# Kernel optimization log

Hardware: AMD Instinct MI355X
Metric: run time of the kernel (lower is better)

## Reference

```python
import jax, jax.numpy as jnp
import numpy as np

H, BOTTLENECK, TOPK = 2048, 64, 128
TAU, EPS = 1.0, 1e-20

def setup_inputs() -> dict:
    key = jax.random.key(0)
    ks = jax.random.split(key, 7)
    B, T = 4, 4096
    x = jax.random.normal(ks[0], (B, T, H), dtype=jnp.float32)
    Wd = jax.random.normal(ks[1], (H, BOTTLENECK), dtype=jnp.float32) / np.sqrt(H)
    bd = jax.random.normal(ks[2], (BOTTLENECK,), dtype=jnp.float32) * 0.01
    Wu = jax.random.normal(ks[3], (BOTTLENECK, H), dtype=jnp.float32) / np.sqrt(BOTTLENECK)
    bu = jax.random.normal(ks[4], (H,), dtype=jnp.float32) * 0.01
    Wg = jax.random.normal(ks[5], (H,), dtype=jnp.float32) / np.sqrt(H)
    bg = jax.random.normal(ks[6], (), dtype=jnp.float32) * 0.01
    return {"x": x, "Wd": Wd, "bd": bd, "Wu": Wu, "bu": bu, "Wg": Wg, "bg": bg}

def reference(x, Wd, bd, Wu, bu, Wg, bg):
    B, T, _ = x.shape
    k = max(1, min(T, TOPK))
    # gate logits: Linear(H,1).squeeze(-1) -> [B, T]
    logits = jnp.einsum('bth,h->bt', x, Wg) + bg
    # gumbel noise (fixed key for determinism; non-differentiated like torch)
    U = jax.random.uniform(jax.random.key(42), logits.shape, dtype=logits.dtype)
    g = -jnp.log(-jnp.log(U + EPS) + EPS)
    probs = jax.nn.softmax((logits + g) / TAU, axis=-1)            # [B, T]
    topk_idx = jax.lax.top_k(logits, k)[1]                          # [B, k]
    hard = jnp.zeros_like(logits).at[jnp.arange(B)[:, None], topk_idx].set(1.0)
    mask = jax.lax.stop_gradient(hard - probs) + probs              # straight-through
    # bottleneck adapter
    delta = jnp.maximum(x @ Wd + bd, 0.0) @ Wu + bu                 # [B, T, H]
    return x + delta * mask[..., None]
```

## Files before the change

kernel.cpp:

```cpp
#include <hip/hip_runtime.h>
#include <hip/hip_bf16.h>

#define H 2048
#define BN 64
#define TT 4096
#define BB 4
#define KK 128
#define CP_BLOCKS 2048
#define RPB 4

typedef float vf4 __attribute__((ext_vector_type(4)));

__global__ __launch_bounds__(256, 8) void copy_logits_kernel(
    const float* __restrict__ x, const float* __restrict__ Wg,
    float* __restrict__ out, float* __restrict__ lpart, int nhalf) {
    const int lane = threadIdx.x & 63;
    const int wv   = (blockIdx.x * 256 + threadIdx.x) >> 6;
    const int nw   = CP_BLOCKS * 4;
    const vf4* w4  = (const vf4*)Wg + (size_t)(wv & 1) * 256;

    for (int hr = wv; hr < nhalf; hr += 2 * nw) {
        const int hr2 = hr + nw;
        const vf4* xs0 = (const vf4*)x + (size_t)hr * 256;
        const vf4* xs1 = (const vf4*)x + (size_t)hr2 * 256;
        vf4* os0 = (vf4*)out + (size_t)hr * 256;
        vf4* os1 = (vf4*)out + (size_t)hr2 * 256;

        vf4 a[4], b[4];
#pragma unroll
        for (int i = 0; i < 4; ++i) a[i] = __builtin_nontemporal_load(&xs0[lane + 64 * i]);
#pragma unroll
        for (int i = 0; i < 4; ++i) b[i] = __builtin_nontemporal_load(&xs1[lane + 64 * i]);

        float s0 = 0.f, s1 = 0.f, s2 = 0.f, s3 = 0.f;
        float t0 = 0.f, t1 = 0.f, t2 = 0.f, t3 = 0.f;
#pragma unroll
        for (int i = 0; i < 4; ++i) {
            vf4 w = w4[lane + 64 * i];
            __builtin_nontemporal_store(a[i], &os0[lane + 64 * i]);
            s0 = fmaf(a[i].x, w.x, s0); s1 = fmaf(a[i].y, w.y, s1);
            s2 = fmaf(a[i].z, w.z, s2); s3 = fmaf(a[i].w, w.w, s3);
        }
#pragma unroll
        for (int i = 0; i < 4; ++i) {
            vf4 w = w4[lane + 64 * i];
            __builtin_nontemporal_store(b[i], &os1[lane + 64 * i]);
            t0 = fmaf(b[i].x, w.x, t0); t1 = fmaf(b[i].y, w.y, t1);
            t2 = fmaf(b[i].z, w.z, t2); t3 = fmaf(b[i].w, w.w, t3);
        }
        float accA = (s0 + s1) + (s2 + s3);
        float accB = (t0 + t1) + (t2 + t3);
#pragma unroll
        for (int off = 32; off > 0; off >>= 1) {
            accA += __shfl_down(accA, off);
            accB += __shfl_down(accB, off);
        }
        if (lane == 0) { lpart[hr] = accA; lpart[hr2] = accB; }
    }
}

__global__ __launch_bounds__(256) void topk_idx_kernel(
    const float* __restrict__ lpart, int* __restrict__ idxlist) {
    __shared__ unsigned keys[TT];
    __shared__ int wsum[4];
    __shared__ int gtp[256], eqp[256];
    const int tid = threadIdx.x;
    const int b   = blockIdx.x;
    const float* lp = lpart + (size_t)b * TT * 2;

    for (int i = tid; i < TT; i += 256) {
        float v = lp[2 * i] + lp[2 * i + 1];
        unsigned u = __float_as_uint(v);
        keys[i] = (u & 0x80000000u) ? ~u : (u | 0x80000000u);
    }
    __syncthreads();

    unsigned prefix = 0;
    int k = KK;
    for (int bit = 31; bit >= 0; --bit) {
        unsigned ref = (prefix >> bit) | 1u;
        int c = 0;
        for (int i = tid; i < TT; i += 256) c += ((keys[i] >> bit) == ref);
#pragma unroll
        for (int off = 32; off > 0; off >>= 1) c += __shfl_down(c, off);
        if ((tid & 63) == 0) wsum[tid >> 6] = c;
        __syncthreads();
        int total = wsum[0] + wsum[1] + wsum[2] + wsum[3];
        __syncthreads();
        if (total >= k) prefix |= (1u << bit);
        else            k -= total;
    }

    const int per = TT / 256, i0 = tid * per, i1 = i0 + per;
    int cgt = 0, ceq = 0;
    for (int i = i0; i < i1; ++i) {
        cgt += (keys[i] > prefix);
        ceq += (keys[i] == prefix);
    }
    gtp[tid] = cgt; eqp[tid] = ceq;
    __syncthreads();
    if (tid == 0) {
        int sg = 0, se = 0;
        for (int t = 0; t < 256; ++t) {
            int a = gtp[t]; gtp[t] = sg; sg += a;
            int c = eqp[t]; eqp[t] = se; se += c;
        }
        wsum[0] = sg;
    }
    __syncthreads();
    const int total_gt = wsum[0];
    const int need_eq  = KK - total_gt;
    int g = gtp[tid], e = eqp[tid];
    int* dst = idxlist + b * KK;
    for (int i = i0; i < i1; ++i) {
        if (keys[i] > prefix)       dst[g++] = b * TT + i;
        else if (keys[i] == prefix) { if (e < need_eq) dst[total_gt + e] = b * TT + i; e++; }
    }
}

__global__ __launch_bounds__(512) void adapter_kernel(
    const float* __restrict__ x, const float* __restrict__ Wd,
    const float* __restrict__ bd, const float* __restrict__ Wu,
    const float* __restrict__ bu, const int* __restrict__ idxlist,
    float* __restrict__ out) {
    __shared__ float hp[8][RPB][BN];
    __shared__ float hs[RPB][BN];
    const int tid  = threadIdx.x;
    const int lane = tid & 63;
    const int g    = tid >> 6;

    int rows[RPB];
#pragma unroll
    for (int r = 0; r < RPB; ++r) rows[r] = idxlist[blockIdx.x * RPB + r];

    float xr[RPB][4];
#pragma unroll
    for (int r = 0; r < RPB; ++r) {
        const float* p = x + (size_t)rows[r] * H + g * 256 + lane;
#pragma unroll
        for (int k = 0; k < 4; ++k) xr[r][k] = p[k * 64];
    }

    float acc[RPB];
#pragma unroll
    for (int r = 0; r < RPB; ++r) acc[r] = 0.f;
    const float* wdp = Wd + (size_t)(g * 256) * BN + lane;
#pragma unroll
    for (int k = 0; k < 4; ++k) {
#pragma unroll 8
        for (int l = 0; l < 64; ++l) {
            float wv = wdp[(size_t)(k * 64 + l) * BN];
#pragma unroll
            for (int r = 0; r < RPB; ++r)
                acc[r] = fmaf(__int_as_float(__builtin_amdgcn_readlane(
                                  __float_as_int(xr[r][k]), l)), wv, acc[r]);
        }
    }
#pragma unroll
    for (int r = 0; r < RPB; ++r) hp[g][r][lane] = acc[r];
    __syncthreads();

    if (tid < RPB * BN) {
        int r = tid >> 6, jj = tid & 63;
        float v = bd[jj];
#pragma unroll
        for (int gg = 0; gg < 8; ++gg) v += hp[gg][r][jj];
        hs[r][jj] = v > 0.f ? v : 0.f;
    }
    __syncthreads();

    const float4* Wu4 = (const float4*)Wu;
    float4 yb = ((const float4*)bu)[tid];
    float4 y[RPB];
#pragma unroll
    for (int r = 0; r < RPB; ++r) y[r] = yb;
    for (int jj = 0; jj < BN; ++jj) {
        float4 wv = Wu4[(size_t)jj * (H / 4) + tid];
#pragma unroll
        for (int r = 0; r < RPB; ++r) {
            float h = hs[r][jj];
            y[r].x = fmaf(h, wv.x, y[r].x); y[r].y = fmaf(h, wv.y, y[r].y);
            y[r].z = fmaf(h, wv.z, y[r].z); y[r].w = fmaf(h, wv.w, y[r].w);
        }
    }
#pragma unroll
    for (int r = 0; r < RPB; ++r) {
        const float4* xr4 = (const float4*)(x + (size_t)rows[r] * H);
        float4*       o4  = (float4*)(out + (size_t)rows[r] * H);
        float4 xa = xr4[tid];
        o4[tid] = make_float4(xa.x + y[r].x, xa.y + y[r].y,
                              xa.z + y[r].z, xa.w + y[r].w);
    }
}

extern "C" void kernel_launch(void* const* d_in, const int* in_sizes, int n_in,
                              void* d_out, int out_size, void* d_ws, size_t ws_size,
                              hipStream_t stream) {
    const float* x  = (const float*)d_in[0];
    const float* Wd = (const float*)d_in[1];
    const float* bd = (const float*)d_in[2];
    const float* Wu = (const float*)d_in[3];
    const float* bu = (const float*)d_in[4];
    const float* Wg = (const float*)d_in[5];
    float* out = (float*)d_out;

    const int nrows = in_sizes[0] / H;
    const int nhalf = nrows * 2;
    float* lpart   = (float*)d_ws;
    int*   idxlist = (int*)((char*)d_ws + (size_t)nhalf * sizeof(float));

    copy_logits_kernel<<<CP_BLOCKS, 256, 0, stream>>>(x, Wg, out, lpart, nhalf);
    topk_idx_kernel<<<BB, 256, 0, stream>>>(lpart, idxlist);
    adapter_kernel<<<(BB * KK) / RPB, 512, 0, stream>>>(x, Wd, bd, Wu, bu, idxlist, out);
}
```

Measured before the change: 101.5 us.

## Split fused copy+logits pass into separate logits and copy kernels

The kernel that both copied x to out and computed gate logits is split in two. A read-only logits kernel now uses normal cached loads and keeps the Wg slice in registers. A separate writer kernel, launched after top-k, streams x to out with nontemporal stores. The aim is to shorten the logits pass and rely on x staying in the large last-level cache for the second read. The cost is an extra full read of x (about 134 MB) and one more kernel launch.

```diff
diff --git a/kernel.cpp b/kernel.cpp
--- a/kernel.cpp
+++ b/kernel.cpp
@@ -7,46 +7,40 @@
 #define BB 4
 #define KK 128
 #define CP_BLOCKS 2048
+#define WR_BLOCKS 2048
 #define RPB 4
 
 typedef float vf4 __attribute__((ext_vector_type(4)));
 
-__global__ __launch_bounds__(256, 8) void copy_logits_kernel(
+__global__ __launch_bounds__(256, 8) void logits_kernel(
     const float* __restrict__ x, const float* __restrict__ Wg,
-    float* __restrict__ out, float* __restrict__ lpart, int nhalf) {
+    float* __restrict__ lpart, int nhalf) {
     const int lane = threadIdx.x & 63;
     const int wv   = (blockIdx.x * 256 + threadIdx.x) >> 6;
     const int nw   = CP_BLOCKS * 4;
     const vf4* w4  = (const vf4*)Wg + (size_t)(wv & 1) * 256;
+    vf4 w[4];
+#pragma unroll
+    for (int i = 0; i < 4; ++i) w[i] = w4[lane + 64 * i];
 
     for (int hr = wv; hr < nhalf; hr += 2 * nw) {
         const int hr2 = hr + nw;
         const vf4* xs0 = (const vf4*)x + (size_t)hr * 256;
         const vf4* xs1 = (const vf4*)x + (size_t)hr2 * 256;
-        vf4* os0 = (vf4*)out + (size_t)hr * 256;
-        vf4* os1 = (vf4*)out + (size_t)hr2 * 256;
-
         vf4 a[4], b[4];
 #pragma unroll
-        for (int i = 0; i < 4; ++i) a[i] = __builtin_nontemporal_load(&xs0[lane + 64 * i]);
-#pragma unroll
-        for (int i = 0; i < 4; ++i) b[i] = __builtin_nontemporal_load(&xs1[lane + 64 * i]);
+        for (int i = 0; i < 4; ++i) a[i] = xs0[lane + 64 * i];
+#pragma unroll
+        for (int i = 0; i < 4; ++i) b[i] = xs1[lane + 64 * i];
 
         float s0 = 0.f, s1 = 0.f, s2 = 0.f, s3 = 0.f;
         float t0 = 0.f, t1 = 0.f, t2 = 0.f, t3 = 0.f;
 #pragma unroll
         for (int i = 0; i < 4; ++i) {
-            vf4 w = w4[lane + 64 * i];
-            __builtin_nontemporal_store(a[i], &os0[lane + 64 * i]);
-            s0 = fmaf(a[i].x, w.x, s0); s1 = fmaf(a[i].y, w.y, s1);
-            s2 = fmaf(a[i].z, w.z, s2); s3 = fmaf(a[i].w, w.w, s3);
-        }
-#pragma unroll
-        for (int i = 0; i < 4; ++i) {
-            vf4 w = w4[lane + 64 * i];
-            __builtin_nontemporal_store(b[i], &os1[lane + 64 * i]);
-            t0 = fmaf(b[i].x, w.x, t0); t1 = fmaf(b[i].y, w.y, t1);
-            t2 = fmaf(b[i].z, w.z, t2); t3 = fmaf(b[i].w, w.w, t3);
+            s0 = fmaf(a[i].x, w[i].x, s0); s1 = fmaf(a[i].y, w[i].y, s1);
+            s2 = fmaf(a[i].z, w[i].z, s2); s3 = fmaf(a[i].w, w[i].w, s3);
+            t0 = fmaf(b[i].x, w[i].x, t0); t1 = fmaf(b[i].y, w[i].y, t1);
+            t2 = fmaf(b[i].z, w[i].z, t2); t3 = fmaf(b[i].w, w[i].w, t3);
         }
         float accA = (s0 + s1) + (s2 + s3);
         float accB = (t0 + t1) + (t2 + t3);
@@ -115,6 +109,23 @@
     for (int i = i0; i < i1; ++i) {
         if (keys[i] > prefix)       dst[g++] = b * TT + i;
         else if (keys[i] == prefix) { if (e < need_eq) dst[total_gt + e] = b * TT + i; e++; }
+    }
+}
+
+__global__ __launch_bounds__(256, 8) void writer_kernel(
+    const float* __restrict__ x, float* __restrict__ out, int n4) {
+    const vf4* xv = (const vf4*)x;
+    vf4*       ov = (vf4*)out;
+    const int stride = WR_BLOCKS * 256;
+    for (int i = blockIdx.x * 256 + threadIdx.x; i < n4; i += 4 * stride) {
+        vf4 a0 = xv[i];
+        vf4 a1 = xv[i + stride];
+        vf4 a2 = xv[i + 2 * stride];
+        vf4 a3 = xv[i + 3 * stride];
+        __builtin_nontemporal_store(a0, &ov[i]);
+        __builtin_nontemporal_store(a1, &ov[i + stride]);
+        __builtin_nontemporal_store(a2, &ov[i + 2 * stride]);
+        __builtin_nontemporal_store(a3, &ov[i + 3 * stride]);
     }
 }
 
@@ -206,10 +217,12 @@
 
     const int nrows = in_sizes[0] / H;
     const int nhalf = nrows * 2;
+    const int n4    = nrows * (H / 4);
     float* lpart   = (float*)d_ws;
     int*   idxlist = (int*)((char*)d_ws + (size_t)nhalf * sizeof(float));
 
-    copy_logits_kernel<<<CP_BLOCKS, 256, 0, stream>>>(x, Wg, out, lpart, nhalf);
+    logits_kernel<<<CP_BLOCKS, 256, 0, stream>>>(x, Wg, lpart, nhalf);
     topk_idx_kernel<<<BB, 256, 0, stream>>>(lpart, idxlist);
+    writer_kernel<<<WR_BLOCKS, 256, 0, stream>>>(x, out, n4);
     adapter_kernel<<<(BB * KK) / RPB, 512, 0, stream>>>(x, Wd, bd, Wu, bu, idxlist, out);
 }
```

Result: slower. 122.2 us (+20.5%).

## Split adapter into down-proj and up-proj kernels, hoist gate weights, drop nontemporal loads

Applied to the files above, without the earlier changes.

The fused adapter kernel is split in two. h_kernel computes the relu bottleneck activations into a workspace buffer, and up_kernel computes the up-projection with twice as many 256-thread blocks, each covering half the columns. This raises parallelism in the up-projection phase at the cost of an extra launch and a global round trip for h. The copy/logits kernel also hoists the Wg loads out of the loop into registers and switches x loads from nontemporal to normal loads.

```diff
diff --git a/kernel.cpp b/kernel.cpp
--- a/kernel.cpp
+++ b/kernel.cpp
@@ -18,6 +18,9 @@
     const int wv   = (blockIdx.x * 256 + threadIdx.x) >> 6;
     const int nw   = CP_BLOCKS * 4;
     const vf4* w4  = (const vf4*)Wg + (size_t)(wv & 1) * 256;
+    vf4 w[4];
+#pragma unroll
+    for (int i = 0; i < 4; ++i) w[i] = w4[lane + 64 * i];
 
     for (int hr = wv; hr < nhalf; hr += 2 * nw) {
         const int hr2 = hr + nw;
@@ -28,25 +31,23 @@
 
         vf4 a[4], b[4];
 #pragma unroll
-        for (int i = 0; i < 4; ++i) a[i] = __builtin_nontemporal_load(&xs0[lane + 64 * i]);
-#pragma unroll
-        for (int i = 0; i < 4; ++i) b[i] = __builtin_nontemporal_load(&xs1[lane + 64 * i]);
+        for (int i = 0; i < 4; ++i) a[i] = xs0[lane + 64 * i];
+#pragma unroll
+        for (int i = 0; i < 4; ++i) b[i] = xs1[lane + 64 * i];
 
         float s0 = 0.f, s1 = 0.f, s2 = 0.f, s3 = 0.f;
         float t0 = 0.f, t1 = 0.f, t2 = 0.f, t3 = 0.f;
 #pragma unroll
         for (int i = 0; i < 4; ++i) {
-            vf4 w = w4[lane + 64 * i];
             __builtin_nontemporal_store(a[i], &os0[lane + 64 * i]);
-            s0 = fmaf(a[i].x, w.x, s0); s1 = fmaf(a[i].y, w.y, s1);
-            s2 = fmaf(a[i].z, w.z, s2); s3 = fmaf(a[i].w, w.w, s3);
+            s0 = fmaf(a[i].x, w[i].x, s0); s1 = fmaf(a[i].y, w[i].y, s1);
+            s2 = fmaf(a[i].z, w[i].z, s2); s3 = fmaf(a[i].w, w[i].w, s3);
         }
 #pragma unroll
         for (int i = 0; i < 4; ++i) {
-            vf4 w = w4[lane + 64 * i];
             __builtin_nontemporal_store(b[i], &os1[lane + 64 * i]);
-            t0 = fmaf(b[i].x, w.x, t0); t1 = fmaf(b[i].y, w.y, t1);
-            t2 = fmaf(b[i].z, w.z, t2); t3 = fmaf(b[i].w, w.w, t3);
+            t0 = fmaf(b[i].x, w[i].x, t0); t1 = fmaf(b[i].y, w[i].y, t1);
+            t2 = fmaf(b[i].z, w[i].z, t2); t3 = fmaf(b[i].w, w[i].w, t3);
         }
         float accA = (s0 + s1) + (s2 + s3);
         float accB = (t0 + t1) + (t2 + t3);
@@ -118,13 +119,11 @@
     }
 }
 
-__global__ __launch_bounds__(512) void adapter_kernel(
+__global__ __launch_bounds__(512) void h_kernel(
     const float* __restrict__ x, const float* __restrict__ Wd,
-    const float* __restrict__ bd, const float* __restrict__ Wu,
-    const float* __restrict__ bu, const int* __restrict__ idxlist,
-    float* __restrict__ out) {
+    const float* __restrict__ bd, const int* __restrict__ idxlist,
+    float* __restrict__ hbuf) {
     __shared__ float hp[8][RPB][BN];
-    __shared__ float hs[RPB][BN];
     const int tid  = threadIdx.x;
     const int lane = tid & 63;
     const int g    = tid >> 6;
@@ -165,17 +164,32 @@
         float v = bd[jj];
 #pragma unroll
         for (int gg = 0; gg < 8; ++gg) v += hp[gg][r][jj];
-        hs[r][jj] = v > 0.f ? v : 0.f;
-    }
-    __syncthreads();
-
-    const float4* Wu4 = (const float4*)Wu;
-    float4 yb = ((const float4*)bu)[tid];
+        hbuf[(size_t)(blockIdx.x * RPB + r) * BN + jj] = v > 0.f ? v : 0.f;
+    }
+}
+
+__global__ __launch_bounds__(256) void up_kernel(
+    const float* __restrict__ x, const float* __restrict__ Wu,
+    const float* __restrict__ bu, const int* __restrict__ idxlist,
+    const float* __restrict__ hbuf, float* __restrict__ out) {
+    __shared__ float hs[RPB][BN];
+    const int tid   = threadIdx.x;
+    const int rg    = blockIdx.x >> 1;
+    const int obase = (blockIdx.x & 1) * (H / 2);
+
+    int rows[RPB];
+#pragma unroll
+    for (int r = 0; r < RPB; ++r) rows[r] = idxlist[rg * RPB + r];
+    if (tid < RPB * BN) ((float*)hs)[tid] = hbuf[(size_t)rg * RPB * BN + tid];
+    __syncthreads();
+
+    const int col = obase + 4 * tid;
+    float4 yb = *(const float4*)(bu + col);
     float4 y[RPB];
 #pragma unroll
     for (int r = 0; r < RPB; ++r) y[r] = yb;
     for (int jj = 0; jj < BN; ++jj) {
-        float4 wv = Wu4[(size_t)jj * (H / 4) + tid];
+        float4 wv = *(const float4*)(Wu + (size_t)jj * H + col);
 #pragma unroll
         for (int r = 0; r < RPB; ++r) {
             float h = hs[r][jj];
@@ -185,11 +199,10 @@
     }
 #pragma unroll
     for (int r = 0; r < RPB; ++r) {
-        const float4* xr4 = (const float4*)(x + (size_t)rows[r] * H);
-        float4*       o4  = (float4*)(out + (size_t)rows[r] * H);
-        float4 xa = xr4[tid];
-        o4[tid] = make_float4(xa.x + y[r].x, xa.y + y[r].y,
-                              xa.z + y[r].z, xa.w + y[r].w);
+        float4 xa = *(const float4*)(x + (size_t)rows[r] * H + col);
+        *(float4*)(out + (size_t)rows[r] * H + col) =
+            make_float4(xa.x + y[r].x, xa.y + y[r].y,
+                        xa.z + y[r].z, xa.w + y[r].w);
     }
 }
 
@@ -206,10 +219,14 @@
 
     const int nrows = in_sizes[0] / H;
     const int nhalf = nrows * 2;
-    float* lpart   = (float*)d_ws;
-    int*   idxlist = (int*)((char*)d_ws + (size_t)nhalf * sizeof(float));
+    char* ws = (char*)d_ws;
+    float* lpart   = (float*)ws;
+    int*   idxlist = (int*)(ws + (size_t)nhalf * sizeof(float));
+    float* hbuf    = (float*)(ws + (size_t)nhalf * sizeof(float)
+                                 + (size_t)BB * KK * sizeof(int));
 
     copy_logits_kernel<<<CP_BLOCKS, 256, 0, stream>>>(x, Wg, out, lpart, nhalf);
     topk_idx_kernel<<<BB, 256, 0, stream>>>(lpart, idxlist);
-    adapter_kernel<<<(BB * KK) / RPB, 512, 0, stream>>>(x, Wd, bd, Wu, bu, idxlist, out);
-}
+    h_kernel<<<(BB * KK) / RPB, 512, 0, stream>>>(x, Wd, bd, idxlist, hbuf);
+    up_kernel<<<2 * (BB * KK) / RPB, 256, 0, stream>>>(x, Wu, bu, idxlist, hbuf, out);
+}
```

Measured after the change: 100.3 us. No clear change (-1.1%).
